# Kernel optimization log

Hardware: AMD Instinct MI355X
Metric: run time of the kernel (lower is better)

The kernel has to match this reference:

```python
import jax, jax.numpy as jnp
import numpy as np


def _normalized_adj(A):
    # get_a: d = 0.5*I, a = off-diagonal ones + A, a2 = d @ a @ d
    off = jnp.array([[0., 1., 1.], [1., 0., 1.], [1., 1., 0.]], dtype=A.dtype)
    a = off + A
    d = 0.5 * jnp.eye(3, dtype=A.dtype)
    return d @ a @ d  # [3,3]


def setup_inputs() -> dict:
    key = jax.random.key(0)
    k1, k2 = jax.random.split(key)
    B = 8192
    x = jax.random.normal(k1, (B, 3, 10), dtype=jnp.float32)
    A = jnp.eye(3, dtype=jnp.float32)  # get_A() returns identity; Parameter init
    stdv = 1.0 / np.sqrt(10.0)
    W = jax.random.uniform(k2, (10, 10), dtype=jnp.float32, minval=-stdv, maxval=stdv)
    return {"x": x, "A": A, "W": W}


def reference(x, A, W):
    # adjacency is detached in the torch forward
    adj = jax.lax.stop_gradient(_normalized_adj(A))  # [3,3], shared across batch
    # GraphConvolution: adj @ (x @ W)
    support = jnp.einsum('bnf,fo->bno', x, W)          # [B,3,10]
    h = jnp.einsum('nm,bmo->bno', adj, support)        # [B,3,10]
    # permute -> [B,10,3]; AvgPool1d(2) on length 3 -> length 1: mean of nodes 0,1
    pooled = 0.5 * (h[:, 0, :] + h[:, 1, :])           # [B,10]
    # ScaleDotProductAttention over the batch axis
    score = jax.nn.softmax(pooled @ pooled.T, axis=-1)  # [B,B]
    v = score @ pooled                                  # [B,10]
    return v
```

## Files before the change

### kernel.cpp

```cpp
#include <hip/hip_runtime.h>
#include <math.h>

#define BROWS 8192
#define F 10
#define TJ 256
#define QPITCH 20
#define APITCH (TJ + 8)
#define LOG2E 1.44269504088896340736f

#if __has_builtin(__builtin_amdgcn_exp2f)
#define EXP2F(x) __builtin_amdgcn_exp2f(x)
#else
#define EXP2F(x) exp2f(x)
#endif

typedef _Float16 half4 __attribute__((ext_vector_type(4)));
typedef float floatx4 __attribute__((ext_vector_type(4)));

__device__ __forceinline__ uint32_t pack2(_Float16 a, _Float16 b) {
    union { _Float16 h[2]; uint32_t u; } x;
    x.h[0] = a; x.h[1] = b;
    return x.u;
}

__global__ void pooled_kernel(const float* __restrict__ x,
                              const float* __restrict__ A,
                              const float* __restrict__ W,
                              float* __restrict__ pooled) {
    int b = blockIdx.x * blockDim.x + threadIdx.x;
    if (b >= BROWS) return;

    float c0 = 0.125f * (1.0f + A[0] + A[3]);
    float c1 = 0.125f * (1.0f + A[1] + A[4]);
    float c2 = 0.125f * (2.0f + A[2] + A[5]);

    const float2* xb = (const float2*)(x + (size_t)b * 3 * F);
    float xv[3 * F];
#pragma unroll
    for (int k = 0; k < 15; ++k) {
        float2 t = xb[k];
        xv[2 * k] = t.x; xv[2 * k + 1] = t.y;
    }

    float y[F];
#pragma unroll
    for (int f = 0; f < F; ++f)
        y[f] = c0 * xv[f] + c1 * xv[F + f] + c2 * xv[2 * F + f];

#pragma unroll
    for (int o = 0; o < F; ++o) {
        float acc = 0.0f;
#pragma unroll
        for (int f = 0; f < F; ++f)
            acc = fmaf(y[f], W[f * F + o], acc);
        pooled[(size_t)b * F + o] = acc;
    }
}

__global__ void attn_kernel(const float* __restrict__ pooled,
                            float* __restrict__ part,
                            float* __restrict__ out,
                            int S, int writeOut) {
    __shared__ _Float16 qrow[TJ * QPITCH];
    __shared__ _Float16 augT[16 * APITCH];

    const int tid  = threadIdx.x;
    const int wave = tid >> 6;
    const int lane = tid & 63;
    const int m    = lane & 15;
    const int quad = lane >> 4;

    const int sIdx   = blockIdx.x % S;
    const int rowBlk = blockIdx.x / S;
    const int irow   = rowBlk * 64 + wave * 16 + m;

    half4 b1;
#pragma unroll
    for (int idx = 0; idx < 4; ++idx) {
        int f = quad * 4 + idx;
        float v = (f < F) ? pooled[(size_t)irow * F + f] * LOG2E : 0.0f;
        b1[idx] = (_Float16)v;
    }

    for (int e = tid; e < 6 * APITCH; e += 256) {
        int n = 10 + e / APITCH;
        int j = e % APITCH;
        augT[n * APITCH + j] = (n == 10) ? (_Float16)1.0f : (_Float16)0.0f;
    }

    const int jext   = BROWS / S;
    const int j0base = sIdx * jext;

    floatx4 acc0 = {0.f, 0.f, 0.f, 0.f};
    floatx4 acc1 = {0.f, 0.f, 0.f, 0.f};

    for (int r = 0; r < jext / TJ; ++r) {
        const int j0g = j0base + r * TJ;
        __syncthreads();
        {
            const float2* src = (const float2*)(pooled + (size_t)(j0g + tid) * F);
            float2 q0 = src[0], q1 = src[1], q2 = src[2], q3 = src[3], q4 = src[4];
            _Float16 h0 = (_Float16)q0.x, h1 = (_Float16)q0.y;
            _Float16 h2 = (_Float16)q1.x, h3 = (_Float16)q1.y;
            _Float16 h4 = (_Float16)q2.x, h5 = (_Float16)q2.y;
            _Float16 h6 = (_Float16)q3.x, h7 = (_Float16)q3.y;
            _Float16 h8 = (_Float16)q4.x, h9 = (_Float16)q4.y;

            uint32_t* qr = (uint32_t*)&qrow[tid * QPITCH];
            qr[0] = pack2(h0, h1); qr[1] = pack2(h2, h3); qr[2] = pack2(h4, h5);
            qr[3] = pack2(h6, h7); qr[4] = pack2(h8, h9);
            qr[5] = 0u; qr[6] = 0u; qr[7] = 0u;

            augT[0 * APITCH + tid] = h0; augT[1 * APITCH + tid] = h1;
            augT[2 * APITCH + tid] = h2; augT[3 * APITCH + tid] = h3;
            augT[4 * APITCH + tid] = h4; augT[5 * APITCH + tid] = h5;
            augT[6 * APITCH + tid] = h6; augT[7 * APITCH + tid] = h7;
            augT[8 * APITCH + tid] = h8; augT[9 * APITCH + tid] = h9;
        }
        __syncthreads();

#pragma unroll
        for (int jt = 0; jt < TJ / 16; jt += 2) {
            {
                const int jb = jt * 16;
                half4 a1 = *(const half4*)((const char*)qrow +
                           (((jb + m) * QPITCH + quad * 4) * 2));
                floatx4 d1 = __builtin_amdgcn_mfma_f32_16x16x16f16(
                    a1, b1, (floatx4){0.f, 0.f, 0.f, 0.f}, 0, 0, 0);
                half4 a2;
                a2[0] = (_Float16)EXP2F(d1[0]); a2[1] = (_Float16)EXP2F(d1[1]);
                a2[2] = (_Float16)EXP2F(d1[2]); a2[3] = (_Float16)EXP2F(d1[3]);
                half4 ag = *(const half4*)((const char*)augT +
                           ((m * APITCH + jb + quad * 4) * 2));
                acc0 = __builtin_amdgcn_mfma_f32_16x16x16f16(ag, a2, acc0, 0, 0, 0);
            }
            {
                const int jb = (jt + 1) * 16;
                half4 a1 = *(const half4*)((const char*)qrow +
                           (((jb + m) * QPITCH + quad * 4) * 2));
                floatx4 d1 = __builtin_amdgcn_mfma_f32_16x16x16f16(
                    a1, b1, (floatx4){0.f, 0.f, 0.f, 0.f}, 0, 0, 0);
                half4 a2;
                a2[0] = (_Float16)EXP2F(d1[0]); a2[1] = (_Float16)EXP2F(d1[1]);
                a2[2] = (_Float16)EXP2F(d1[2]); a2[3] = (_Float16)EXP2F(d1[3]);
                half4 ag = *(const half4*)((const char*)augT +
                           ((m * APITCH + jb + quad * 4) * 2));
                acc1 = __builtin_amdgcn_mfma_f32_16x16x16f16(ag, a2, acc1, 0, 0, 0);
            }
        }
    }

    floatx4 acc = acc0 + acc1;

    if (writeOut) {
        float l = __shfl(acc[2], 32 + m, 64);
        float inv = 1.0f / l;
        float2* o = (float2*)(out + (size_t)irow * F);
        if (quad == 0) {
            o[0] = make_float2(acc[0] * inv, acc[1] * inv);
            o[1] = make_float2(acc[2] * inv, acc[3] * inv);
        } else if (quad == 1) {
            o[2] = make_float2(acc[0] * inv, acc[1] * inv);
            o[3] = make_float2(acc[2] * inv, acc[3] * inv);
        } else if (quad == 2) {
            o[4] = make_float2(acc[0] * inv, acc[1] * inv);
        }
    } else {
        if (quad < 3) {
            floatx4* dst = (floatx4*)(part +
                ((size_t)sIdx * BROWS + irow) * 12 + quad * 4);
            *dst = acc;
        }
    }
}

__global__ void reduce_kernel(const float* __restrict__ part,
                              float* __restrict__ out, int S) {
    int i = blockIdx.x * blockDim.x + threadIdx.x;
    if (i >= BROWS) return;
    floatx4 v0 = {0.f,0.f,0.f,0.f}, v1 = {0.f,0.f,0.f,0.f}, v2 = {0.f,0.f,0.f,0.f};
    for (int s = 0; s < S; ++s) {
        const floatx4* p = (const floatx4*)(part + ((size_t)s * BROWS + i) * 12);
        v0 += p[0]; v1 += p[1]; v2 += p[2];
    }
    float inv = 1.0f / v2[2];
    float2* o = (float2*)(out + (size_t)i * F);
    o[0] = make_float2(v0[0] * inv, v0[1] * inv);
    o[1] = make_float2(v0[2] * inv, v0[3] * inv);
    o[2] = make_float2(v1[0] * inv, v1[1] * inv);
    o[3] = make_float2(v1[2] * inv, v1[3] * inv);
    o[4] = make_float2(v2[0] * inv, v2[1] * inv);
}

extern "C" void kernel_launch(void* const* d_in, const int* in_sizes, int n_in,
                              void* d_out, int out_size, void* d_ws, size_t ws_size,
                              hipStream_t stream) {
    const float* x = (const float*)d_in[0];
    const float* A = (const float*)d_in[1];
    const float* W = (const float*)d_in[2];
    float* out = (float*)d_out;

    float* pooled = (float*)d_ws;
    size_t pooledBytes = (size_t)BROWS * F * sizeof(float);
    size_t partOff = (pooledBytes + 255) & ~(size_t)255;
    float* part = (float*)((char*)d_ws + partOff);
    size_t avail = ws_size > partOff ? ws_size - partOff : 0;

    int S = 1;
    for (int c = 8; c >= 2; c >>= 1) {
        if ((size_t)c * BROWS * 12 * sizeof(float) <= avail) { S = c; break; }
    }

    pooled_kernel<<<BROWS / 256, 256, 0, stream>>>(x, A, W, pooled);
    if (S >= 2) {
        attn_kernel<<<128 * S, 256, 0, stream>>>(pooled, part, out, S, 0);
        reduce_kernel<<<BROWS / 256, 256, 0, stream>>>(part, out, S);
    } else {
        attn_kernel<<<128, 256, 0, stream>>>(pooled, part, out, 1, 1);
    }
}
```

Before: 77.01 us.

## Split key axis across waves in-block and drop the separate reduce kernel

Restructures attention so each 512-thread block owns 16 query rows and its 8 waves split the key tiles, combining the partial sums in shared memory. This replaces the split-S grid plus global partial buffer and separate reduce kernel with one in-block reduction. It also prefetches the next key tile into registers during compute, uses packed round-toward-zero fp16 conversion after exp2, and launches pooled_kernel with 64-thread blocks. The grid grows to 512 blocks, but every block re-stages all 8192 keys through LDS, which adds LDS traffic and many barriers.

```diff
diff --git a/kernel.cpp b/kernel.cpp
--- a/kernel.cpp
+++ b/kernel.cpp
@@ -3,7 +3,7 @@
 
 #define BROWS 8192
 #define F 10
-#define TJ 256
+#define TJ 512
 #define QPITCH 20
 #define APITCH (TJ + 8)
 #define LOG2E 1.44269504088896340736f
@@ -15,7 +15,22 @@
 #endif
 
 typedef _Float16 half4 __attribute__((ext_vector_type(4)));
+typedef __fp16 fp16x2 __attribute__((ext_vector_type(2)));
 typedef float floatx4 __attribute__((ext_vector_type(4)));
+
+__device__ __forceinline__ half4 exp4_to_h4(float a, float b, float c, float d) {
+#if __has_builtin(__builtin_amdgcn_cvt_pkrtz)
+    union { fp16x2 h2[2]; half4 h4; } u;
+    u.h2[0] = __builtin_amdgcn_cvt_pkrtz(EXP2F(a), EXP2F(b));
+    u.h2[1] = __builtin_amdgcn_cvt_pkrtz(EXP2F(c), EXP2F(d));
+    return u.h4;
+#else
+    half4 r;
+    r[0] = (_Float16)EXP2F(a); r[1] = (_Float16)EXP2F(b);
+    r[2] = (_Float16)EXP2F(c); r[3] = (_Float16)EXP2F(d);
+    return r;
+#endif
+}
 
 __device__ __forceinline__ uint32_t pack2(_Float16 a, _Float16 b) {
     union { _Float16 h[2]; uint32_t u; } x;
@@ -58,21 +73,17 @@
 }
 
 __global__ void attn_kernel(const float* __restrict__ pooled,
-                            float* __restrict__ part,
-                            float* __restrict__ out,
-                            int S, int writeOut) {
-    __shared__ _Float16 qrow[TJ * QPITCH];
-    __shared__ _Float16 augT[16 * APITCH];
+                            float* __restrict__ out) {
+    __shared__ __align__(16) _Float16 qrow[TJ * QPITCH];
+    __shared__ __align__(16) _Float16 augT[16 * APITCH];
+    __shared__ __align__(16) float red[8 * 16 * 12];
 
     const int tid  = threadIdx.x;
     const int wave = tid >> 6;
     const int lane = tid & 63;
     const int m    = lane & 15;
     const int quad = lane >> 4;
-
-    const int sIdx   = blockIdx.x % S;
-    const int rowBlk = blockIdx.x / S;
-    const int irow   = rowBlk * 64 + wave * 16 + m;
+    const int irow = blockIdx.x * 16 + m;
 
     half4 b1;
 #pragma unroll
@@ -82,29 +93,29 @@
         b1[idx] = (_Float16)v;
     }
 
-    for (int e = tid; e < 6 * APITCH; e += 256) {
+    for (int e = tid; e < 6 * APITCH; e += 512) {
         int n = 10 + e / APITCH;
         int j = e % APITCH;
         augT[n * APITCH + j] = (n == 10) ? (_Float16)1.0f : (_Float16)0.0f;
     }
 
-    const int jext   = BROWS / S;
-    const int j0base = sIdx * jext;
-
     floatx4 acc0 = {0.f, 0.f, 0.f, 0.f};
     floatx4 acc1 = {0.f, 0.f, 0.f, 0.f};
 
-    for (int r = 0; r < jext / TJ; ++r) {
-        const int j0g = j0base + r * TJ;
+    float2 s0, s1, s2, s3, s4;
+    {
+        const float2* src = (const float2*)(pooled + (size_t)tid * F);
+        s0 = src[0]; s1 = src[1]; s2 = src[2]; s3 = src[3]; s4 = src[4];
+    }
+
+    for (int t = 0; t < BROWS / TJ; ++t) {
         __syncthreads();
         {
-            const float2* src = (const float2*)(pooled + (size_t)(j0g + tid) * F);
-            float2 q0 = src[0], q1 = src[1], q2 = src[2], q3 = src[3], q4 = src[4];
-            _Float16 h0 = (_Float16)q0.x, h1 = (_Float16)q0.y;
-            _Float16 h2 = (_Float16)q1.x, h3 = (_Float16)q1.y;
-            _Float16 h4 = (_Float16)q2.x, h5 = (_Float16)q2.y;
-            _Float16 h6 = (_Float16)q3.x, h7 = (_Float16)q3.y;
-            _Float16 h8 = (_Float16)q4.x, h9 = (_Float16)q4.y;
+            _Float16 h0 = (_Float16)s0.x, h1 = (_Float16)s0.y;
+            _Float16 h2 = (_Float16)s1.x, h3 = (_Float16)s1.y;
+            _Float16 h4 = (_Float16)s2.x, h5 = (_Float16)s2.y;
+            _Float16 h6 = (_Float16)s3.x, h7 = (_Float16)s3.y;
+            _Float16 h8 = (_Float16)s4.x, h9 = (_Float16)s4.y;
 
             uint32_t* qr = (uint32_t*)&qrow[tid * QPITCH];
             qr[0] = pack2(h0, h1); qr[1] = pack2(h2, h3); qr[2] = pack2(h4, h5);
@@ -119,77 +130,44 @@
         }
         __syncthreads();
 
+        if (t + 1 < BROWS / TJ) {
+            const float2* src = (const float2*)(pooled +
+                                (size_t)((t + 1) * TJ + tid) * F);
+            s0 = src[0]; s1 = src[1]; s2 = src[2]; s3 = src[3]; s4 = src[4];
+        }
+
 #pragma unroll
-        for (int jt = 0; jt < TJ / 16; jt += 2) {
-            {
-                const int jb = jt * 16;
-                half4 a1 = *(const half4*)((const char*)qrow +
-                           (((jb + m) * QPITCH + quad * 4) * 2));
-                floatx4 d1 = __builtin_amdgcn_mfma_f32_16x16x16f16(
-                    a1, b1, (floatx4){0.f, 0.f, 0.f, 0.f}, 0, 0, 0);
-                half4 a2;
-                a2[0] = (_Float16)EXP2F(d1[0]); a2[1] = (_Float16)EXP2F(d1[1]);
-                a2[2] = (_Float16)EXP2F(d1[2]); a2[3] = (_Float16)EXP2F(d1[3]);
-                half4 ag = *(const half4*)((const char*)augT +
-                           ((m * APITCH + jb + quad * 4) * 2));
+        for (int c = 0; c < 4; ++c) {
+            const int jb = wave * 64 + c * 16;
+            half4 a1 = *(const half4*)&qrow[(jb + m) * QPITCH + quad * 4];
+            floatx4 d1 = __builtin_amdgcn_mfma_f32_16x16x16f16(
+                a1, b1, (floatx4){0.f, 0.f, 0.f, 0.f}, 0, 0, 0);
+            half4 a2 = exp4_to_h4(d1[0], d1[1], d1[2], d1[3]);
+            half4 ag = *(const half4*)&augT[m * APITCH + jb + quad * 4];
+            if (c & 1)
+                acc1 = __builtin_amdgcn_mfma_f32_16x16x16f16(ag, a2, acc1, 0, 0, 0);
+            else
                 acc0 = __builtin_amdgcn_mfma_f32_16x16x16f16(ag, a2, acc0, 0, 0, 0);
-            }
-            {
-                const int jb = (jt + 1) * 16;
-                half4 a1 = *(const half4*)((const char*)qrow +
-                           (((jb + m) * QPITCH + quad * 4) * 2));
-                floatx4 d1 = __builtin_amdgcn_mfma_f32_16x16x16f16(
-                    a1, b1, (floatx4){0.f, 0.f, 0.f, 0.f}, 0, 0, 0);
-                half4 a2;
-                a2[0] = (_Float16)EXP2F(d1[0]); a2[1] = (_Float16)EXP2F(d1[1]);
-                a2[2] = (_Float16)EXP2F(d1[2]); a2[3] = (_Float16)EXP2F(d1[3]);
-                half4 ag = *(const half4*)((const char*)augT +
-                           ((m * APITCH + jb + quad * 4) * 2));
-                acc1 = __builtin_amdgcn_mfma_f32_16x16x16f16(ag, a2, acc1, 0, 0, 0);
-            }
         }
     }
 
     floatx4 acc = acc0 + acc1;
 
-    if (writeOut) {
-        float l = __shfl(acc[2], 32 + m, 64);
-        float inv = 1.0f / l;
-        float2* o = (float2*)(out + (size_t)irow * F);
-        if (quad == 0) {
-            o[0] = make_float2(acc[0] * inv, acc[1] * inv);
-            o[1] = make_float2(acc[2] * inv, acc[3] * inv);
-        } else if (quad == 1) {
-            o[2] = make_float2(acc[0] * inv, acc[1] * inv);
-            o[3] = make_float2(acc[2] * inv, acc[3] * inv);
-        } else if (quad == 2) {
-            o[4] = make_float2(acc[0] * inv, acc[1] * inv);
+    if (quad < 3)
+        *(floatx4*)&red[(wave * 16 + m) * 12 + quad * 4] = acc;
+    __syncthreads();
+
+    if (tid < 160) {
+        const int i16 = tid / 10;
+        const int f   = tid % 10;
+        float sum = 0.0f, l = 0.0f;
+#pragma unroll
+        for (int w = 0; w < 8; ++w) {
+            sum += red[(w * 16 + i16) * 12 + f];
+            l   += red[(w * 16 + i16) * 12 + 10];
         }
-    } else {
-        if (quad < 3) {
-            floatx4* dst = (floatx4*)(part +
-                ((size_t)sIdx * BROWS + irow) * 12 + quad * 4);
-            *dst = acc;
-        }
+        out[(size_t)(blockIdx.x * 16 + i16) * F + f] = sum / l;
     }
-}
-
-__global__ void reduce_kernel(const float* __restrict__ part,
-                              float* __restrict__ out, int S) {
-    int i = blockIdx.x * blockDim.x + threadIdx.x;
-    if (i >= BROWS) return;
-    floatx4 v0 = {0.f,0.f,0.f,0.f}, v1 = {0.f,0.f,0.f,0.f}, v2 = {0.f,0.f,0.f,0.f};
-    for (int s = 0; s < S; ++s) {
-        const floatx4* p = (const floatx4*)(part + ((size_t)s * BROWS + i) * 12);
-        v0 += p[0]; v1 += p[1]; v2 += p[2];
-    }
-    float inv = 1.0f / v2[2];
-    float2* o = (float2*)(out + (size_t)i * F);
-    o[0] = make_float2(v0[0] * inv, v0[1] * inv);
-    o[1] = make_float2(v0[2] * inv, v0[3] * inv);
-    o[2] = make_float2(v1[0] * inv, v1[1] * inv);
-    o[3] = make_float2(v1[2] * inv, v1[3] * inv);
-    o[4] = make_float2(v2[0] * inv, v2[1] * inv);
 }
 
 extern "C" void kernel_launch(void* const* d_in, const int* in_sizes, int n_in,
@@ -199,23 +177,8 @@
     const float* A = (const float*)d_in[1];
     const float* W = (const float*)d_in[2];
     float* out = (float*)d_out;
+    float* pooled = (float*)d_ws;
 
-    float* pooled = (float*)d_ws;
-    size_t pooledBytes = (size_t)BROWS * F * sizeof(float);
-    size_t partOff = (pooledBytes + 255) & ~(size_t)255;
-    float* part = (float*)((char*)d_ws + partOff);
-    size_t avail = ws_size > partOff ? ws_size - partOff : 0;
-
-    int S = 1;
-    for (int c = 8; c >= 2; c >>= 1) {
-        if ((size_t)c * BROWS * 12 * sizeof(float) <= avail) { S = c; break; }
-    }
-
-    pooled_kernel<<<BROWS / 256, 256, 0, stream>>>(x, A, W, pooled);
-    if (S >= 2) {
-        attn_kernel<<<128 * S, 256, 0, stream>>>(pooled, part, out, S, 0);
-        reduce_kernel<<<BROWS / 256, 256, 0, stream>>>(part, out, S);
-    } else {
-        attn_kernel<<<128, 256, 0, stream>>>(pooled, part, out, 1, 1);
-    }
+    pooled_kernel<<<BROWS / 64, 64, 0, stream>>>(x, A, W, pooled);
+    attn_kernel<<<BROWS / 16, 512, 0, stream>>>(pooled, out);
 }
```

Result: no change. 77.98 us (+1.3%).
